# Kernel tuning notes

Measured on AMD Instinct MI355X. Metric: run time of the kernel, lower is better.

The kernel has to match this reference:

```python
import math
import jax, jax.numpy as jnp
import numpy as np

N, L, C_IMG, D, FF, H, NL, V = 2, 1024, 512, 512, 2048, 8, 4, 8000
EPS_ATTN = 1e-6
EPS_LN = 1e-5


def pos_enc(position, channels):
    # position: (N, L, 1) float. channels assumed even here (256 / 512).
    num = channels // 2
    log_inc = math.log(10000.0) / (num - 1)
    inv = jnp.exp(jnp.arange(num, dtype=position.dtype) * -log_inc)
    st = position * inv.reshape(1, 1, -1)  # (N, L, num)
    return jnp.concatenate([jnp.sin(st), jnp.cos(st)], -1)


def layer_norm(x, s, b):
    m = jnp.mean(x, -1, keepdims=True)
    v = jnp.mean((x - m) ** 2, -1, keepdims=True)
    return (x - m) / jnp.sqrt(v + EPS_LN) * s + b


def causal_linear_attention(x, mask, Wq, bq, Wk, bk, Wv, bv, Wo, bo):
    # x: (N, L, D), mask: (N, L, 1)
    n, l, d = x.shape
    q = (x @ Wq + bq).reshape(n, l, H, -1)
    k = (x @ Wk + bk).reshape(n, l, H, -1)
    v = (x @ Wv + bv).reshape(n, l, H, -1)
    Q = jax.nn.elu(q) + 1.0                       # elu feature map
    K = (jax.nn.elu(k) + 1.0) * mask[:, :, :, None]
    K_cum = jnp.cumsum(K, axis=1)                 # (N, L, H, dk)
    Z = 1.0 / (jnp.einsum('nlhd,nlhd->nlh', Q, K_cum) + EPS_ATTN)
    KV = jnp.cumsum(K[..., :, None] * v[..., None, :], axis=1)  # (N, L, H, dk, dv)
    out = jnp.einsum('nlhd,nlhde->nlhe', Q, KV) * Z[..., None]
    return out.reshape(n, l, d) @ Wo + bo


def encoder_layer(x, mask, p):
    (Wq, bq, Wk, bk, Wv, bv, Wo, bo, W1, b1, W2, b2, s1, be1, s2, be2) = p
    x = x + causal_linear_attention(x, mask, Wq, bq, Wk, bk, Wv, bv, Wo, bo)
    x = layer_norm(x, s1, be1)
    y = jax.nn.gelu(x @ W1 + b1, approximate=False) @ W2 + b2
    return layer_norm(x + y, s2, be2)


def setup_inputs() -> dict:
    key = jax.random.key(0)
    ks = iter(jax.random.split(key, 64))

    def p(shape):
        return jax.random.normal(next(ks), shape, dtype=jnp.float32) * 0.02

    x_img = jax.random.normal(next(ks), (N, L, C_IMG), dtype=jnp.float32)
    x_txt = jax.random.randint(next(ks), (N, L), 0, V)
    pos = jnp.broadcast_to(jnp.arange(L, dtype=jnp.float32)[None, :, None], (N, L, 1))
    pos_r = jnp.floor(pos / 32.0)
    pos_c = jnp.mod(pos, 32.0)
    pos_t = pos
    first_half = (jnp.arange(L) < L // 2).astype(jnp.float32)[None, :, None]
    mask_img = jnp.broadcast_to(first_half, (N, L, 1))
    mask_txt = 1.0 - mask_img

    inp = dict(x_img=x_img, x_txt=x_txt, mask_img=mask_img, mask_txt=mask_txt,
               pos_r=pos_r, pos_c=pos_c, pos_t=pos_t,
               W_ei=p((C_IMG, D)), b_ei=jnp.zeros((D,)),
               emb_txt=p((V, D)),
               Wq=p((NL, D, D)), bq=jnp.zeros((NL, D)),
               Wk=p((NL, D, D)), bk=jnp.zeros((NL, D)),
               Wv=p((NL, D, D)), bv=jnp.zeros((NL, D)),
               Wo=p((NL, D, D)), bo=jnp.zeros((NL, D)),
               W1=p((NL, D, FF)), b1=jnp.zeros((NL, FF)),
               W2=p((NL, FF, D)), b2=jnp.zeros((NL, D)),
               ln1_s=jnp.ones((NL, D)), ln1_b=jnp.zeros((NL, D)),
               ln2_s=jnp.ones((NL, D)), ln2_b=jnp.zeros((NL, D)),
               W_pi=p((D, C_IMG)), b_pi=jnp.zeros((C_IMG,)),
               W_pt=p((D, V)), b_pt=jnp.zeros((V,)))
    return inp


def reference(x_img, x_txt, mask_img, mask_txt, pos_r, pos_c, pos_t,
              W_ei, b_ei, emb_txt,
              Wq, bq, Wk, bk, Wv, bv, Wo, bo, W1, b1, W2, b2,
              ln1_s, ln1_b, ln2_s, ln2_b, W_pi, b_pi, W_pt, b_pt):
    x_mask = mask_img + mask_txt  # (N, L, 1)
    # image embedding
    half = D // 2
    x_pos = jnp.concatenate([pos_enc(pos_r, half), pos_enc(pos_c, D - half)], -1)
    x_emb_img = ((x_img @ W_ei + b_ei) + x_pos) * mask_img
    # text embedding
    x_emb_txt = (emb_txt[x_txt] + pos_enc(pos_t, D)) * mask_txt
    x = x_emb_img + x_emb_txt
    for i in range(NL):
        p = (Wq[i], bq[i], Wk[i], bk[i], Wv[i], bv[i], Wo[i], bo[i],
             W1[i], b1[i], W2[i], b2[i], ln1_s[i], ln1_b[i], ln2_s[i], ln2_b[i])
        x = encoder_layer(x, x_mask, p)
    logit_img = x @ W_pi + b_pi
    logit_txt = x @ W_pt + b_pt
    return (logit_img, logit_txt)
```

## Files before the change

### kernel.cpp

```cpp
#include <hip/hip_runtime.h>
#include <hip/hip_bf16.h>
#include <math.h>

#define NB 2
#define LSEQ 1024
#define DM 512
#define FFD 2048
#define NHEAD 8
#define DKH 64
#define NLAYER 4
#define VOCAB 8000
#define NCHUNK 16
#define NROWS (NB * LSEQ)
#define QS 1536
#define NHEADCAT 8512
#define NHEADPAD 8576

#define OP_NONE 0
#define OP_GELU 2
#define OP_QKV  3
#define OP_PART 4
#define OP_HEAD 5

typedef __attribute__((ext_vector_type(8))) short short8;
typedef __attribute__((ext_vector_type(4))) float f32x4;
typedef __hip_bfloat16 bf16;

__device__ __forceinline__ void cast_tile(
    const float* __restrict__ s, bf16* __restrict__ d, int K, int N,
    int n0, int k0, int tid)
{
    __shared__ float tile[32][33];
    const int r  = tid >> 3;
    const int c4 = (tid & 7) * 4;
    const int n  = n0 + c4;
    float4 v = make_float4(0.f, 0.f, 0.f, 0.f);
    if (n < N)
        v = *(const float4*)(s + (size_t)(k0 + r) * N + n);
    tile[r][c4 + 0] = v.x; tile[r][c4 + 1] = v.y;
    tile[r][c4 + 2] = v.z; tile[r][c4 + 3] = v.w;
    __syncthreads();
    const int nr = tid >> 3;
    const int kc = (tid & 7) * 4;
    bf16 o[4];
    o[0] = __float2bfloat16(tile[kc + 0][nr]);
    o[1] = __float2bfloat16(tile[kc + 1][nr]);
    o[2] = __float2bfloat16(tile[kc + 2][nr]);
    o[3] = __float2bfloat16(tile[kc + 3][nr]);
    *(unsigned long long*)(d + (size_t)(n0 + nr) * K + k0 + kc) =
        *(const unsigned long long*)o;
    __syncthreads();
}

#define CO_QKVO 0
#define CO_W1   4096
#define CO_W2   8192
#define CO_WEI  12288
#define CO_WPI  12544
#define CO_WPT  12800
#define CO_XIMG 16832
#define CO_QKVB 17856
#define CO_HB   17860
#define CO_END  17894

__global__ __launch_bounds__(256) void setup_all(
    const float* __restrict__ Wq, const float* __restrict__ Wk,
    const float* __restrict__ Wv, const float* __restrict__ Wo,
    const float* __restrict__ W1, const float* __restrict__ W2,
    const float* __restrict__ Wei, const float* __restrict__ Wpi,
    const float* __restrict__ Wpt,
    bf16* __restrict__ QKVt, bf16* __restrict__ Wot,
    bf16* __restrict__ W1t, bf16* __restrict__ W2t,
    bf16* __restrict__ Weit, bf16* __restrict__ Whead,
    const float* __restrict__ x_img, bf16* __restrict__ ximgh,
    const float* __restrict__ bq, const float* __restrict__ bk,
    const float* __restrict__ bv, float* __restrict__ qkvB,
    const float* __restrict__ bpi, const float* __restrict__ bpt,
    float* __restrict__ hb)
{
    const int id = blockIdx.x;
    const int tid = threadIdx.x;

    if (id < CO_W1) {
        const int rel = id;
        const int z = rel >> 8, t = rel & 255;
        const int layer = z >> 2, which = z & 3;
        const float* src = (which == 0 ? Wq : which == 1 ? Wk : which == 2 ? Wv : Wo)
                           + (size_t)layer * 262144;
        bf16* dst = (which < 3)
            ? (QKVt + (size_t)layer * 786432 + (size_t)which * 262144)
            : (Wot + (size_t)layer * 262144);
        cast_tile(src, dst, 512, 512, (t & 15) * 32, (t >> 4) * 32, tid);
    } else if (id < CO_W2) {
        const int rel = id - CO_W1;
        const int z = rel >> 10, t = rel & 1023;
        cast_tile(W1 + (size_t)z * 1048576, W1t + (size_t)z * 1048576,
                  512, 2048, (t & 63) * 32, (t >> 6) * 32, tid);
    } else if (id < CO_WEI) {
        const int rel = id - CO_W2;
        const int z = rel >> 10, t = rel & 1023;
        cast_tile(W2 + (size_t)z * 1048576, W2t + (size_t)z * 1048576,
                  2048, 512, (t & 15) * 32, (t >> 4) * 32, tid);
    } else if (id < CO_WPI) {
        const int t = id - CO_WEI;
        cast_tile(Wei, Weit, 512, 512, (t & 15) * 32, (t >> 4) * 32, tid);
    } else if (id < CO_WPT) {
        const int t = id - CO_WPI;
        cast_tile(Wpi, Whead, 512, 512, (t & 15) * 32, (t >> 4) * 32, tid);
    } else if (id < CO_XIMG) {
        const int t = id - CO_WPT;
        cast_tile(Wpt, Whead + 262144, 512, VOCAB,
                  (t % 252) * 32, (t / 252) * 32, tid);
    } else if (id < CO_QKVB) {
        const int i = (id - CO_XIMG) * 256 + tid;
        const float4 v = *(const float4*)(x_img + (size_t)i * 4);
        ximgh[(size_t)i * 4 + 0] = __float2bfloat16(v.x);
        ximgh[(size_t)i * 4 + 1] = __float2bfloat16(v.y);
        ximgh[(size_t)i * 4 + 2] = __float2bfloat16(v.z);
        ximgh[(size_t)i * 4 + 3] = __float2bfloat16(v.w);
    } else if (id < CO_HB) {
        const int z = id - CO_QKVB;
        for (int j = tid; j < QS; j += 256) {
            float v;
            if (j < 512)       v = bq[z * DM + j];
            else if (j < 1024) v = bk[z * DM + j - 512];
            else               v = bv[z * DM + j - 1024];
            qkvB[z * QS + j] = v;
        }
    } else {
        const int j = (id - CO_HB) * 256 + tid;
        if (j < NHEADPAD)
            hb[j] = (j < 512) ? bpi[j] : (j < NHEADCAT ? bpt[j - 512] : 0.f);
    }
}

template<int BM, int BN>
__global__ __launch_bounds__(256) void gemm16(
    const bf16* __restrict__ A, const bf16* __restrict__ Bt,
    const float* __restrict__ bias, const float* __restrict__ res,
    float* __restrict__ outF, float* __restrict__ outF2,
    bf16* __restrict__ outH,
    int M, int K, int Nout, int op, int kslab)
{
    constexpr int WM = BM / 2, WN = BN / 2, MI = WM / 16, NI = WN / 16;
    constexpr int LA = BM / 64, LB = BN / 64;
    constexpr int NL = LA + LB;
    __shared__ bf16 As[3][BM * 32];
    __shared__ bf16 Bs[3][BN * 32];
    const int tid = threadIdx.x;
    const int lane = tid & 63;
    const int wave = tid >> 6;
    const int wm = (wave >> 1) * WM, wn = (wave & 1) * WN;

    int bxi = blockIdx.x, byi = blockIdx.y;
    if (op == OP_HEAD) {
        const int gx = gridDim.x;
        const int nwg = gx * gridDim.y;
        int flat = byi * gx + bxi;
        const int q = nwg >> 3, r = nwg & 7;
        const int xcd = flat & 7, lid = flat >> 3;
        flat = (xcd < r ? xcd * (q + 1) : r * (q + 1) + (xcd - r) * q) + lid;
        bxi = flat % gx;
        byi = flat / gx;
    }
    const int bm = (op == OP_HEAD ? bxi : blockIdx.y) * BM;
    const int bn = (op == OP_HEAD ? byi : blockIdx.x) * BN;
    const int l16 = lane & 15, quad = lane >> 4;

    const int rA = tid >> 2;
    const int c8 = (tid & 3) << 3;

    f32x4 acc[MI][NI];
    #pragma unroll
    for (int i = 0; i < MI; ++i)
        #pragma unroll
        for (int j = 0; j < NI; ++j) acc[i][j] = (f32x4){0.f, 0.f, 0.f, 0.f};

    const bf16* gA = A  + (size_t)(bm + rA) * K + c8;
    const bf16* gB = Bt + (size_t)(bn + rA) * K + c8;
    const int ldsWaveOff = wave * 1024;

    const int kStart = blockIdx.z * kslab;
    const int kEnd = kStart + kslab;

    auto stage = [&](int buf, int k0) {
        #pragma unroll
        for (int i = 0; i < LA; ++i)
            __builtin_amdgcn_global_load_lds(
                (const __attribute__((address_space(1))) void*)(gA + (size_t)i * 64 * K + k0),
                (__attribute__((address_space(3))) void*)((char*)As[buf] + i * 4096 + ldsWaveOff),
                16, 0, 0);
        #pragma unroll
        for (int i = 0; i < LB; ++i)
            __builtin_amdgcn_global_load_lds(
                (const __attribute__((address_space(1))) void*)(gB + (size_t)i * 64 * K + k0),
                (__attribute__((address_space(3))) void*)((char*)Bs[buf] + i * 4096 + ldsWaveOff),
                16, 0, 0);
    };

    stage(0, kStart);
    if (kStart + 32 < kEnd) stage(1, kStart + 32);
    int cur = 0;
    for (int k0 = kStart; k0 < kEnd; k0 += 32) {
        const int k2 = k0 + 64;
        if (k2 < kEnd) {
            int nb = cur + 2; if (nb >= 3) nb -= 3;
            stage(nb, k2);
            asm volatile("s_waitcnt vmcnt(%0)" :: "n"(2 * NL) : "memory");
        } else if (k0 + 32 < kEnd) {
            asm volatile("s_waitcnt vmcnt(%0)" :: "n"(NL) : "memory");
        } else {
            asm volatile("s_waitcnt vmcnt(0)" ::: "memory");
        }
        __builtin_amdgcn_s_barrier();
        short8 a[MI], b[NI];
        #pragma unroll
        for (int i = 0; i < MI; ++i)
            a[i] = *(const short8*)(As[cur] + (size_t)(wm + i * 16 + l16) * 32 + quad * 8);
        #pragma unroll
        for (int j = 0; j < NI; ++j)
            b[j] = *(const short8*)(Bs[cur] + (size_t)(wn + j * 16 + l16) * 32 + quad * 8);
        #pragma unroll
        for (int i = 0; i < MI; ++i)
            #pragma unroll
            for (int j = 0; j < NI; ++j)
                acc[i][j] = __builtin_amdgcn_mfma_f32_16x16x32_bf16(
                    a[i], b[j], acc[i][j], 0, 0, 0);
        __builtin_amdgcn_s_barrier();
        ++cur; if (cur >= 3) cur -= 3;
    }

    if (op == OP_PART) {
        float* dst = outF + (size_t)blockIdx.z * (size_t)M * Nout;
        #pragma unroll
        for (int j = 0; j < NI; ++j) {
            const int col = bn + wn + j * 16 + l16;
            #pragma unroll
            for (int i = 0; i < MI; ++i)
                #pragma unroll
                for (int r = 0; r < 4; ++r) {
                    const int row = bm + wm + i * 16 + quad * 4 + r;
                    dst[(size_t)row * Nout + col] = acc[i][j][r];
                }
        }
        return;
    }
    if (op == OP_HEAD) {
        #pragma unroll
        for (int j = 0; j < NI; ++j) {
            const int col = bn + wn + j * 16 + l16;
            const bool cok = (col < NHEADCAT);
            const float bz = cok ? bias[col] : 0.f;
            #pragma unroll
            for (int i = 0; i < MI; ++i)
                #pragma unroll
                for (int r = 0; r < 4; ++r) {
                    const int row = bm + wm + i * 16 + quad * 4 + r;
                    const float v = acc[i][j][r] + bz;
                    if (cok) {
                        if (col < 512) outF[(size_t)row * 512 + col] = v;
                        else           outF2[(size_t)row * VOCAB + (col - 512)] = v;
                    }
                }
        }
        return;
    }

    #pragma unroll
    for (int j = 0; j < NI; ++j) {
        const int col = bn + wn + j * 16 + l16;
        const bool cok = (col < Nout);
        const float bz = cok ? bias[col] : 0.f;
        #pragma unroll
        for (int i = 0; i < MI; ++i) {
            #pragma unroll
            for (int r = 0; r < 4; ++r) {
                const int row = bm + wm + i * 16 + quad * 4 + r;
                float v = acc[i][j][r] + bz;
                if (op == OP_GELU)      v = 0.5f * v * (1.f + erff(v * 0.70710678118654752f));
                else if (op == OP_QKV && col < 1024) v = (v > 0.f) ? v + 1.f : expf(v);
                if (cok) {
                    if (res)  v += res[(size_t)row * Nout + col];
                    if (outF) outF[(size_t)row * Nout + col] = v;
                    if (outH) outH[(size_t)row * Nout + col] = __float2bfloat16(v);
                }
            }
        }
    }
}

__global__ __launch_bounds__(256) void embed_k(
    const float* __restrict__ gI, const int* __restrict__ xt,
    const float* __restrict__ emb,
    const float* __restrict__ mi, const float* __restrict__ mt,
    const float* __restrict__ pr, const float* __restrict__ pc,
    const float* __restrict__ pt, float* __restrict__ X, bf16* __restrict__ Xh)
{
    const int row = blockIdx.x;
    const float prv = pr[row], pcv = pc[row], ptv = pt[row];
    const float miv = mi[row], mtv = mt[row];
    const int tok = xt[row];
    const float LOG1E4 = 9.2103403719761836f;
    const float LI127 = LOG1E4 / 127.f;
    const float LI255 = LOG1E4 / 255.f;

    for (int d = threadIdx.x; d < DM; d += 256) {
        float ip;
        if (d < 128)       ip = sinf(prv * expf(-(float)d * LI127));
        else if (d < 256)  ip = cosf(prv * expf(-(float)(d - 128) * LI127));
        else if (d < 384)  ip = sinf(pcv * expf(-(float)(d - 256) * LI127));
        else               ip = cosf(pcv * expf(-(float)(d - 384) * LI127));
        float tp;
        if (d < 256) tp = sinf(ptv * expf(-(float)d * LI255));
        else         tp = cosf(ptv * expf(-(float)(d - 256) * LI255));
        const float v = miv * (gI[(size_t)row * DM + d] + ip)
                      + mtv * (emb[(size_t)tok * DM + d] + tp);
        X[(size_t)row * DM + d] = v;
        Xh[(size_t)row * DM + d] = __float2bfloat16(v);
    }
}

__global__ __launch_bounds__(256) void ln_red(
    const float* __restrict__ P, int nP,
    const float* __restrict__ bias, const float* __restrict__ res,
    const float* __restrict__ g, const float* __restrict__ b,
    float* __restrict__ out, bf16* __restrict__ outh)
{
    const int row = blockIdx.x;
    const int tid = threadIdx.x;
    const int lane = tid & 63, wv = tid >> 6;
    const size_t base = (size_t)row * DM;
    float x0 = res[base + tid] + bias[tid];
    float x1 = res[base + tid + 256] + bias[tid + 256];
    for (int p = 0; p < nP; ++p) {
        x0 += P[(size_t)p * 1048576 + base + tid];
        x1 += P[(size_t)p * 1048576 + base + tid + 256];
    }
    __shared__ float redA[4];
    __shared__ float redB[4];
    float s = x0 + x1;
    #pragma unroll
    for (int off = 32; off > 0; off >>= 1) s += __shfl_down(s, off);
    if (lane == 0) redA[wv] = s;
    __syncthreads();
    const float mean = (redA[0] + redA[1] + redA[2] + redA[3]) * (1.f / (float)DM);
    const float d0 = x0 - mean, d1 = x1 - mean;
    float v = d0 * d0 + d1 * d1;
    #pragma unroll
    for (int off = 32; off > 0; off >>= 1) v += __shfl_down(v, off);
    if (lane == 0) redB[wv] = v;
    __syncthreads();
    const float var = (redB[0] + redB[1] + redB[2] + redB[3]) * (1.f / (float)DM);
    const float rstd = rsqrtf(var + 1e-5f);
    const float y0 = d0 * rstd * g[tid] + b[tid];
    const float y1 = d1 * rstd * g[tid + 256] + b[tid + 256];
    out[base + tid]        = y0;
    out[base + tid + 256]  = y1;
    outh[base + tid]       = __float2bfloat16(y0);
    outh[base + tid + 256] = __float2bfloat16(y1);
}

__global__ __launch_bounds__(256) void attn_kv(
    const float* __restrict__ Kp, const float* __restrict__ Vp,
    float* __restrict__ S, float* __restrict__ ks)
{
    const int c = blockIdx.x, h = blockIdx.y, n = blockIdx.z;
    const int tid = threadIdx.x;
    __shared__ float sK[64][64], sV[64][64], part[4][64];

    const int lr = tid >> 4;
    const int c4 = (tid & 15) * 4;
    #pragma unroll
    for (int it = 0; it < 4; ++it) {
        const int row = it * 16 + lr;
        const size_t gb = ((size_t)(n * LSEQ + c * 64 + row)) * QS + h * DKH + c4;
        *(float4*)&sK[row][c4] = *(const float4*)(Kp + gb);
        *(float4*)&sV[row][c4] = *(const float4*)(Vp + gb);
    }
    __syncthreads();

    const int e = tid & 63, dq = tid >> 6;
    float s[16] = {};
    for (int l = 0; l < 64; ++l) {
        const float vv = sV[l][e];
        const float4 k0 = *(const float4*)&sK[l][dq * 16 + 0];
        const float4 k1 = *(const float4*)&sK[l][dq * 16 + 4];
        const float4 k2 = *(const float4*)&sK[l][dq * 16 + 8];
        const float4 k3 = *(const float4*)&sK[l][dq * 16 + 12];
        s[0]  = fmaf(k0.x, vv, s[0]);  s[1]  = fmaf(k0.y, vv, s[1]);
        s[2]  = fmaf(k0.z, vv, s[2]);  s[3]  = fmaf(k0.w, vv, s[3]);
        s[4]  = fmaf(k1.x, vv, s[4]);  s[5]  = fmaf(k1.y, vv, s[5]);
        s[6]  = fmaf(k1.z, vv, s[6]);  s[7]  = fmaf(k1.w, vv, s[7]);
        s[8]  = fmaf(k2.x, vv, s[8]);  s[9]  = fmaf(k2.y, vv, s[9]);
        s[10] = fmaf(k2.z, vv, s[10]); s[11] = fmaf(k2.w, vv, s[11]);
        s[12] = fmaf(k3.x, vv, s[12]); s[13] = fmaf(k3.y, vv, s[13]);
        s[14] = fmaf(k3.z, vv, s[14]); s[15] = fmaf(k3.w, vv, s[15]);
    }
    const size_t sb = (((size_t)(n * NHEAD + h)) * NCHUNK + c) * 4096;
    #pragma unroll
    for (int i = 0; i < 16; ++i) S[sb + (size_t)(dq * 16 + i) * 64 + e] = s[i];

    float kp = 0.f;
    #pragma unroll
    for (int i = 0; i < 16; ++i) kp += sK[dq * 16 + i][e];
    part[dq][e] = kp;
    __syncthreads();
    if (tid < 64)
        ks[(((size_t)(n * NHEAD + h)) * NCHUNK + c) * 64 + tid] =
            part[0][tid] + part[1][tid] + part[2][tid] + part[3][tid];
}

__global__ __launch_bounds__(256) void attn_out(
    const float* __restrict__ QKV, const float* __restrict__ S,
    const float* __restrict__ ks, bf16* __restrict__ O)
{
    const int c = blockIdx.x, h = blockIdx.y, n = blockIdx.z;
    const int tid = threadIdx.x;
    __shared__ float sQt[64][64];
    __shared__ float sKt[64][64];
    __shared__ float sV [64][64];
    __shared__ float sS [64][64];
    __shared__ float sPt[64][65];
    __shared__ float skp[64];

    const size_t nhS = ((size_t)(n * NHEAD + h)) * NCHUNK * 4096;
    const size_t nhK = ((size_t)(n * NHEAD + h)) * NCHUNK * 64;

    {
        float4 aS[4] = {};
        for (int cc = 0; cc < c; ++cc) {
            const float* Sc = S + nhS + (size_t)cc * 4096;
            #pragma unroll
            for (int i = 0; i < 4; ++i) {
                const float4 t = *(const float4*)(Sc + i * 1024 + tid * 4);
                aS[i].x += t.x; aS[i].y += t.y; aS[i].z += t.z; aS[i].w += t.w;
            }
        }
        float* sSf = &sS[0][0];
        #pragma unroll
        for (int i = 0; i < 4; ++i)
            *(float4*)(sSf + i * 1024 + tid * 4) = aS[i];
        if (tid < 64) {
            float kp = 0.f;
            for (int cc = 0; cc < c; ++cc) kp += ks[nhK + cc * 64 + tid];
            skp[tid] = kp;
        }
    }

    const int lr = tid >> 4;
    const int c4 = (tid & 15) * 4;
    #pragma unroll
    for (int it = 0; it < 4; ++it) {
        const int row = it * 16 + lr;
        const size_t gb = ((size_t)(n * LSEQ + c * 64 + row)) * QS + h * DKH + c4;
        const float4 q4 = *(const float4*)(QKV + gb);
        const float4 k4 = *(const float4*)(QKV + gb + 512);
        const float4 v4 = *(const float4*)(QKV + gb + 1024);
        sQt[c4 + 0][row] = q4.x; sQt[c4 + 1][row] = q4.y;
        sQt[c4 + 2][row] = q4.z; sQt[c4 + 3][row] = q4.w;
        sKt[c4 + 0][row] = k4.x; sKt[c4 + 1][row] = k4.y;
        sKt[c4 + 2][row] = k4.z; sKt[c4 + 3][row] = k4.w;
        *(float4*)&sV[row][c4] = v4;
    }
    __syncthreads();

    const int m4 = (tid & 15) * 4;
    const int lg = tid >> 4;
    {
        float p[4][4] = {};
        for (int d = 0; d < 64; ++d) {
            const float4 k4 = *(const float4*)&sKt[d][m4];
            const float4 q4 = *(const float4*)&sQt[d][lg * 4];
            p[0][0] = fmaf(q4.x, k4.x, p[0][0]); p[0][1] = fmaf(q4.x, k4.y, p[0][1]);
            p[0][2] = fmaf(q4.x, k4.z, p[0][2]); p[0][3] = fmaf(q4.x, k4.w, p[0][3]);
            p[1][0] = fmaf(q4.y, k4.x, p[1][0]); p[1][1] = fmaf(q4.y, k4.y, p[1][1]);
            p[1][2] = fmaf(q4.y, k4.z, p[1][2]); p[1][3] = fmaf(q4.y, k4.w, p[1][3]);
            p[2][0] = fmaf(q4.z, k4.x, p[2][0]); p[2][1] = fmaf(q4.z, k4.y, p[2][1]);
            p[2][2] = fmaf(q4.z, k4.z, p[2][2]); p[2][3] = fmaf(q4.z, k4.w, p[2][3]);
            p[3][0] = fmaf(q4.w, k4.x, p[3][0]); p[3][1] = fmaf(q4.w, k4.y, p[3][1]);
            p[3][2] = fmaf(q4.w, k4.z, p[3][2]); p[3][3] = fmaf(q4.w, k4.w, p[3][3]);
        }
        #pragma unroll
        for (int jj = 0; jj < 4; ++jj)
            #pragma unroll
            for (int j = 0; j < 4; ++j)
                sPt[m4 + jj][lg * 4 + j] = p[j][jj];
    }
    __syncthreads();

    float acc[4][4] = {};
    float z[4] = {};
    const int lmax = lg * 4 + 3;
    for (int m = 0; m <= lmax; ++m) {
        const float4 v4 = *(const float4*)&sV[m][m4];
        #pragma unroll
        for (int j = 0; j < 4; ++j) {
            const int l = lg * 4 + j;
            float p = sPt[m][l];
            p = (m <= l) ? p : 0.f;
            z[j] += p;
            acc[j][0] = fmaf(p, v4.x, acc[j][0]);
            acc[j][1] = fmaf(p, v4.y, acc[j][1]);
            acc[j][2] = fmaf(p, v4.z, acc[j][2]);
            acc[j][3] = fmaf(p, v4.w, acc[j][3]);
        }
    }
    for (int d = 0; d < 64; ++d) {
        const float4 s4 = *(const float4*)&sS[d][m4];
        const float4 q4 = *(const float4*)&sQt[d][lg * 4];
        const float kp = skp[d];
        z[0] = fmaf(q4.x, kp, z[0]); z[1] = fmaf(q4.y, kp, z[1]);
        z[2] = fmaf(q4.z, kp, z[2]); z[3] = fmaf(q4.w, kp, z[3]);
        acc[0][0] = fmaf(q4.x, s4.x, acc[0][0]); acc[0][1] = fmaf(q4.x, s4.y, acc[0][1]);
        acc[0][2] = fmaf(q4.x, s4.z, acc[0][2]); acc[0][3] = fmaf(q4.x, s4.w, acc[0][3]);
        acc[1][0] = fmaf(q4.y, s4.x, acc[1][0]); acc[1][1] = fmaf(q4.y, s4.y, acc[1][1]);
        acc[1][2] = fmaf(q4.y, s4.z, acc[1][2]); acc[1][3] = fmaf(q4.y, s4.w, acc[1][3]);
        acc[2][0] = fmaf(q4.z, s4.x, acc[2][0]); acc[2][1] = fmaf(q4.z, s4.y, acc[2][1]);
        acc[2][2] = fmaf(q4.z, s4.z, acc[2][2]); acc[2][3] = fmaf(q4.z, s4.w, acc[2][3]);
        acc[3][0] = fmaf(q4.w, s4.x, acc[3][0]); acc[3][1] = fmaf(q4.w, s4.y, acc[3][1]);
        acc[3][2] = fmaf(q4.w, s4.z, acc[3][2]); acc[3][3] = fmaf(q4.w, s4.w, acc[3][3]);
    }
    #pragma unroll
    for (int j = 0; j < 4; ++j) {
        const int l = lg * 4 + j;
        const float rz = 1.f / (z[j] + 1e-6f);
        const size_t ob = ((size_t)(n * LSEQ + c * 64 + l)) * DM + h * DKH + m4;
        O[ob + 0] = __float2bfloat16(acc[j][0] * rz);
        O[ob + 1] = __float2bfloat16(acc[j][1] * rz);
        O[ob + 2] = __float2bfloat16(acc[j][2] * rz);
        O[ob + 3] = __float2bfloat16(acc[j][3] * rz);
    }
}

extern "C" void kernel_launch(void* const* d_in, const int* in_sizes, int n_in,
                              void* d_out, int out_size, void* d_ws, size_t ws_size,
                              hipStream_t stream)
{
    const float* x_img   = (const float*)d_in[0];
    const int*   x_txt   = (const int*)  d_in[1];
    const float* mask_i  = (const float*)d_in[2];
    const float* mask_t  = (const float*)d_in[3];
    const float* pos_r   = (const float*)d_in[4];
    const float* pos_c   = (const float*)d_in[5];
    const float* pos_t   = (const float*)d_in[6];
    const float* W_ei    = (const float*)d_in[7];
    const float* b_ei    = (const float*)d_in[8];
    const float* emb_txt = (const float*)d_in[9];
    const float* Wq      = (const float*)d_in[10];
    const float* bq      = (const float*)d_in[11];
    const float* Wk      = (const float*)d_in[12];
    const float* bk      = (const float*)d_in[13];
    const float* Wv      = (const float*)d_in[14];
    const float* bv      = (const float*)d_in[15];
    const float* Wo      = (const float*)d_in[16];
    const float* bo      = (const float*)d_in[17];
    const float* W1      = (const float*)d_in[18];
    const float* b1      = (const float*)d_in[19];
    const float* W2      = (const float*)d_in[20];
    const float* b2      = (const float*)d_in[21];
    const float* ln1_s   = (const float*)d_in[22];
    const float* ln1_b   = (const float*)d_in[23];
    const float* ln2_s   = (const float*)d_in[24];
    const float* ln2_b   = (const float*)d_in[25];
    const float* W_pi    = (const float*)d_in[26];
    const float* b_pi    = (const float*)d_in[27];
    const float* W_pt    = (const float*)d_in[28];
    const float* b_pt    = (const float*)d_in[29];

    float* ws = (float*)d_ws;
    size_t off = 0;
    auto alloc = [&](size_t nfloats) { float* p = ws + off; off += nfloats; return p; };

    float* Xb   = alloc(1048576);
    float* Pb   = alloc(4194304);
    float* QKVb = alloc(3145728);
    float* Sb   = alloc(1048576);
    float* ksb  = alloc(16384);
    float* qkvB = alloc(4 * QS);
    float* hb   = alloc(8704);
    bf16* Xh    = (bf16*)alloc(524288);
    bf16* Ob    = (bf16*)alloc(524288);
    bf16* Tb    = (bf16*)alloc(2097152);
    bf16* ximgh = (bf16*)alloc(524288);
    bf16* QKVt  = (bf16*)alloc(1572864);
    bf16* Wot   = (bf16*)alloc(524288);
    bf16* W1t   = (bf16*)alloc(2097152);
    bf16* W2t   = (bf16*)alloc(2097152);
    bf16* Weit  = (bf16*)alloc(131072);
    bf16* Whead = (bf16*)alloc(2195456);

    const dim3 blk(256);
    const dim3 gAttn(NCHUNK, NHEAD, NB);

    setup_all<<<dim3(CO_END), blk, 0, stream>>>(
        Wq, Wk, Wv, Wo, W1, W2, W_ei, W_pi, W_pt,
        QKVt, Wot, W1t, W2t, Weit, Whead,
        x_img, ximgh, bq, bk, bv, qkvB, b_pi, b_pt, hb);

    gemm16<64, 64><<<dim3(8, 32), blk, 0, stream>>>(
        ximgh, Weit, b_ei, nullptr, Pb, nullptr, nullptr, NROWS, 512, 512, OP_NONE, 512);
    embed_k<<<NROWS, blk, 0, stream>>>(Pb, x_txt, emb_txt, mask_i, mask_t,
                                       pos_r, pos_c, pos_t, Xb, Xh);

    for (int i = 0; i < NLAYER; ++i) {
        gemm16<64, 128><<<dim3(12, 32), blk, 0, stream>>>(
            Xh, QKVt + (size_t)i * 786432, qkvB + i * QS, nullptr,
            QKVb, nullptr, nullptr, NROWS, 512, QS, OP_QKV, 512);

        attn_kv<<<gAttn, blk, 0, stream>>>(QKVb + 512, QKVb + 1024, Sb, ksb);
        attn_out<<<gAttn, blk, 0, stream>>>(QKVb, Sb, ksb, Ob);

        gemm16<64, 64><<<dim3(8, 32, 2), blk, 0, stream>>>(
            Ob, Wot + (size_t)i * 262144, nullptr, nullptr,
            Pb, nullptr, nullptr, NROWS, 512, 512, OP_PART, 256);
        ln_red<<<NROWS, blk, 0, stream>>>(Pb, 2, bo + (size_t)i * DM, Xb,
                                          ln1_s + (size_t)i * DM,
                                          ln1_b + (size_t)i * DM, Xb, Xh);

        gemm16<64, 128><<<dim3(16, 32), blk, 0, stream>>>(
            Xh, W1t + (size_t)i * 1048576, b1 + (size_t)i * FFD, nullptr,
            nullptr, nullptr, Tb, NROWS, 512, FFD, OP_GELU, 512);
        gemm16<64, 64><<<dim3(8, 32, 4), blk, 0, stream>>>(
            Tb, W2t + (size_t)i * 1048576, nullptr, nullptr,
            Pb, nullptr, nullptr, NROWS, 2048, 512, OP_PART, 512);
        ln_red<<<NROWS, blk, 0, stream>>>(Pb, 4, b2 + (size_t)i * DM, Xb,
                                          ln2_s + (size_t)i * DM,
                                          ln2_b + (size_t)i * DM, Xb, Xh);
    }

    float* out = (float*)d_out;
    gemm16<128, 128><<<dim3(16, 67), blk, 0, stream>>>(
        Xh, Whead, hb, nullptr, out, out + 1048576, nullptr,
        NROWS, 512, NHEADCAT, OP_HEAD, 512);
}
```

Before: 631.1 us.

## Replace 4-wave GEMM with single-wave 64x64 GEMM using swizzled LDS double buffering

Replaces the templated 256-thread GEMM with a single-wave 64x64 tile kernel. It uses a two-buffer LDS pipeline with no workgroup barriers and XOR-swizzled LDS addressing to avoid bank conflicts. Grids are rescaled so every GEMM, including the head, uses 64x64 tiles, giving many more small blocks. This removes barrier overhead and aims for higher occupancy, at the cost of less tile reuse (more global and L2 traffic) for the larger tiles it replaces.

```diff
diff --git a/kernel.cpp b/kernel.cpp
--- a/kernel.cpp
+++ b/kernel.cpp
@@ -134,67 +134,67 @@
     }
 }
 
-template<int BM, int BN>
-__global__ __launch_bounds__(256) void gemm16(
+__global__ __launch_bounds__(64) void wgemm(
     const bf16* __restrict__ A, const bf16* __restrict__ Bt,
     const float* __restrict__ bias, const float* __restrict__ res,
     float* __restrict__ outF, float* __restrict__ outF2,
     bf16* __restrict__ outH,
     int M, int K, int Nout, int op, int kslab)
 {
-    constexpr int WM = BM / 2, WN = BN / 2, MI = WM / 16, NI = WN / 16;
-    constexpr int LA = BM / 64, LB = BN / 64;
-    constexpr int NL = LA + LB;
-    __shared__ bf16 As[3][BM * 32];
-    __shared__ bf16 Bs[3][BN * 32];
-    const int tid = threadIdx.x;
-    const int lane = tid & 63;
-    const int wave = tid >> 6;
-    const int wm = (wave >> 1) * WM, wn = (wave & 1) * WN;
-
-    int bxi = blockIdx.x, byi = blockIdx.y;
+    __shared__ bf16 As[2][64 * 32];
+    __shared__ bf16 Bs[2][64 * 32];
+    const int lane = threadIdx.x;
+    const int l16 = lane & 15, quad = lane >> 4;
+    const int rr = lane >> 2;
+    const int sl = lane & 3;
+
+    int bm, bn;
     if (op == OP_HEAD) {
         const int gx = gridDim.x;
         const int nwg = gx * gridDim.y;
-        int flat = byi * gx + bxi;
+        int flat = blockIdx.y * gx + blockIdx.x;
         const int q = nwg >> 3, r = nwg & 7;
         const int xcd = flat & 7, lid = flat >> 3;
         flat = (xcd < r ? xcd * (q + 1) : r * (q + 1) + (xcd - r) * q) + lid;
-        bxi = flat % gx;
-        byi = flat / gx;
-    }
-    const int bm = (op == OP_HEAD ? bxi : blockIdx.y) * BM;
-    const int bn = (op == OP_HEAD ? byi : blockIdx.x) * BN;
-    const int l16 = lane & 15, quad = lane >> 4;
-
-    const int rA = tid >> 2;
-    const int c8 = (tid & 3) << 3;
-
-    f32x4 acc[MI][NI];
-    #pragma unroll
-    for (int i = 0; i < MI; ++i)
-        #pragma unroll
-        for (int j = 0; j < NI; ++j) acc[i][j] = (f32x4){0.f, 0.f, 0.f, 0.f};
-
-    const bf16* gA = A  + (size_t)(bm + rA) * K + c8;
-    const bf16* gB = Bt + (size_t)(bn + rA) * K + c8;
-    const int ldsWaveOff = wave * 1024;
+        bm = (flat % gx) * 64;
+        bn = (flat / gx) * 64;
+    } else {
+        bm = blockIdx.y * 64;
+        bn = blockIdx.x * 64;
+    }
+
+    f32x4 acc[4][4];
+    #pragma unroll
+    for (int i = 0; i < 4; ++i)
+        #pragma unroll
+        for (int j = 0; j < 4; ++j) acc[i][j] = (f32x4){0.f, 0.f, 0.f, 0.f};
+
+    const int csw = (sl ^ ((rr >> 1) & 3)) << 3;
+    const int rsw = ((quad ^ ((l16 >> 1) & 3)) << 3);
+
+    const bf16* gA[4];
+    const bf16* gB[4];
+    #pragma unroll
+    for (int i = 0; i < 4; ++i) {
+        gA[i] = A  + (size_t)(bm + i * 16 + rr) * K + csw;
+        gB[i] = Bt + (size_t)(bn + i * 16 + rr) * K + csw;
+    }
 
     const int kStart = blockIdx.z * kslab;
     const int kEnd = kStart + kslab;
 
     auto stage = [&](int buf, int k0) {
         #pragma unroll
-        for (int i = 0; i < LA; ++i)
+        for (int i = 0; i < 4; ++i)
             __builtin_amdgcn_global_load_lds(
-                (const __attribute__((address_space(1))) void*)(gA + (size_t)i * 64 * K + k0),
-                (__attribute__((address_space(3))) void*)((char*)As[buf] + i * 4096 + ldsWaveOff),
+                (const __attribute__((address_space(1))) void*)(gA[i] + k0),
+                (__attribute__((address_space(3))) void*)((char*)As[buf] + i * 1024),
                 16, 0, 0);
         #pragma unroll
-        for (int i = 0; i < LB; ++i)
+        for (int i = 0; i < 4; ++i)
             __builtin_amdgcn_global_load_lds(
-                (const __attribute__((address_space(1))) void*)(gB + (size_t)i * 64 * K + k0),
-                (__attribute__((address_space(3))) void*)((char*)Bs[buf] + i * 4096 + ldsWaveOff),
+                (const __attribute__((address_space(1))) void*)(gB[i] + k0),
+                (__attribute__((address_space(3))) void*)((char*)Bs[buf] + i * 1024),
                 16, 0, 0);
     };
 
@@ -202,44 +202,38 @@
     if (kStart + 32 < kEnd) stage(1, kStart + 32);
     int cur = 0;
     for (int k0 = kStart; k0 < kEnd; k0 += 32) {
-        const int k2 = k0 + 64;
-        if (k2 < kEnd) {
-            int nb = cur + 2; if (nb >= 3) nb -= 3;
-            stage(nb, k2);
-            asm volatile("s_waitcnt vmcnt(%0)" :: "n"(2 * NL) : "memory");
-        } else if (k0 + 32 < kEnd) {
-            asm volatile("s_waitcnt vmcnt(%0)" :: "n"(NL) : "memory");
-        } else {
+        if (k0 + 32 < kEnd)
+            asm volatile("s_waitcnt vmcnt(8)" ::: "memory");
+        else
             asm volatile("s_waitcnt vmcnt(0)" ::: "memory");
-        }
-        __builtin_amdgcn_s_barrier();
-        short8 a[MI], b[NI];
-        #pragma unroll
-        for (int i = 0; i < MI; ++i)
-            a[i] = *(const short8*)(As[cur] + (size_t)(wm + i * 16 + l16) * 32 + quad * 8);
-        #pragma unroll
-        for (int j = 0; j < NI; ++j)
-            b[j] = *(const short8*)(Bs[cur] + (size_t)(wn + j * 16 + l16) * 32 + quad * 8);
-        #pragma unroll
-        for (int i = 0; i < MI; ++i)
+        short8 a[4], b[4];
+        #pragma unroll
+        for (int i = 0; i < 4; ++i)
+            a[i] = *(const short8*)(As[cur] + (i * 16 + l16) * 32 + rsw);
+        #pragma unroll
+        for (int j = 0; j < 4; ++j)
+            b[j] = *(const short8*)(Bs[cur] + (j * 16 + l16) * 32 + rsw);
+        asm volatile("s_waitcnt lgkmcnt(0)" ::: "memory");
+        if (k0 + 64 < kEnd) stage(cur, k0 + 64);
+        #pragma unroll
+        for (int i = 0; i < 4; ++i)
             #pragma unroll
-            for (int j = 0; j < NI; ++j)
+            for (int j = 0; j < 4; ++j)
                 acc[i][j] = __builtin_amdgcn_mfma_f32_16x16x32_bf16(
                     a[i], b[j], acc[i][j], 0, 0, 0);
-        __builtin_amdgcn_s_barrier();
-        ++cur; if (cur >= 3) cur -= 3;
+        cur ^= 1;
     }
 
     if (op == OP_PART) {
         float* dst = outF + (size_t)blockIdx.z * (size_t)M * Nout;
         #pragma unroll
-        for (int j = 0; j < NI; ++j) {
-            const int col = bn + wn + j * 16 + l16;
+        for (int j = 0; j < 4; ++j) {
+            const int col = bn + j * 16 + l16;
             #pragma unroll
-            for (int i = 0; i < MI; ++i)
+            for (int i = 0; i < 4; ++i)
                 #pragma unroll
                 for (int r = 0; r < 4; ++r) {
-                    const int row = bm + wm + i * 16 + quad * 4 + r;
+                    const int row = bm + i * 16 + quad * 4 + r;
                     dst[(size_t)row * Nout + col] = acc[i][j][r];
                 }
         }
@@ -247,15 +241,15 @@
     }
     if (op == OP_HEAD) {
         #pragma unroll
-        for (int j = 0; j < NI; ++j) {
-            const int col = bn + wn + j * 16 + l16;
+        for (int j = 0; j < 4; ++j) {
+            const int col = bn + j * 16 + l16;
             const bool cok = (col < NHEADCAT);
             const float bz = cok ? bias[col] : 0.f;
             #pragma unroll
-            for (int i = 0; i < MI; ++i)
+            for (int i = 0; i < 4; ++i)
                 #pragma unroll
                 for (int r = 0; r < 4; ++r) {
-                    const int row = bm + wm + i * 16 + quad * 4 + r;
+                    const int row = bm + i * 16 + quad * 4 + r;
                     const float v = acc[i][j][r] + bz;
                     if (cok) {
                         if (col < 512) outF[(size_t)row * 512 + col] = v;
@@ -267,15 +261,15 @@
     }
 
     #pragma unroll
-    for (int j = 0; j < NI; ++j) {
-        const int col = bn + wn + j * 16 + l16;
+    for (int j = 0; j < 4; ++j) {
+        const int col = bn + j * 16 + l16;
         const bool cok = (col < Nout);
         const float bz = cok ? bias[col] : 0.f;
         #pragma unroll
-        for (int i = 0; i < MI; ++i) {
+        for (int i = 0; i < 4; ++i) {
             #pragma unroll
             for (int r = 0; r < 4; ++r) {
-                const int row = bm + wm + i * 16 + quad * 4 + r;
+                const int row = bm + i * 16 + quad * 4 + r;
                 float v = acc[i][j][r] + bz;
                 if (op == OP_GELU)      v = 0.5f * v * (1.f + erff(v * 0.70710678118654752f));
                 else if (op == OP_QKV && col < 1024) v = (v > 0.f) ? v + 1.f : expf(v);
@@ -590,6 +584,7 @@
     bf16* Whead = (bf16*)alloc(2195456);
 
     const dim3 blk(256);
+    const dim3 wblk(64);
     const dim3 gAttn(NCHUNK, NHEAD, NB);
 
     setup_all<<<dim3(CO_END), blk, 0, stream>>>(
@@ -597,30 +592,30 @@
         QKVt, Wot, W1t, W2t, Weit, Whead,
         x_img, ximgh, bq, bk, bv, qkvB, b_pi, b_pt, hb);
 
-    gemm16<64, 64><<<dim3(8, 32), blk, 0, stream>>>(
+    wgemm<<<dim3(8, 32), wblk, 0, stream>>>(
         ximgh, Weit, b_ei, nullptr, Pb, nullptr, nullptr, NROWS, 512, 512, OP_NONE, 512);
     embed_k<<<NROWS, blk, 0, stream>>>(Pb, x_txt, emb_txt, mask_i, mask_t,
                                        pos_r, pos_c, pos_t, Xb, Xh);
 
     for (int i = 0; i < NLAYER; ++i) {
-        gemm16<64, 128><<<dim3(12, 32), blk, 0, stream>>>(
+        wgemm<<<dim3(24, 32), wblk, 0, stream>>>(
             Xh, QKVt + (size_t)i * 786432, qkvB + i * QS, nullptr,
             QKVb, nullptr, nullptr, NROWS, 512, QS, OP_QKV, 512);
 
         attn_kv<<<gAttn, blk, 0, stream>>>(QKVb + 512, QKVb + 1024, Sb, ksb);
         attn_out<<<gAttn, blk, 0, stream>>>(QKVb, Sb, ksb, Ob);
 
-        gemm16<64, 64><<<dim3(8, 32, 2), blk, 0, stream>>>(
+        wgemm<<<dim3(8, 32, 2), wblk, 0, stream>>>(
             Ob, Wot + (size_t)i * 262144, nullptr, nullptr,
             Pb, nullptr, nullptr, NROWS, 512, 512, OP_PART, 256);
         ln_red<<<NROWS, blk, 0, stream>>>(Pb, 2, bo + (size_t)i * DM, Xb,
                                           ln1_s + (size_t)i * DM,
                                           ln1_b + (size_t)i * DM, Xb, Xh);
 
-        gemm16<64, 128><<<dim3(16, 32), blk, 0, stream>>>(
+        wgemm<<<dim3(32, 32), wblk, 0, stream>>>(
             Xh, W1t + (size_t)i * 1048576, b1 + (size_t)i * FFD, nullptr,
             nullptr, nullptr, Tb, NROWS, 512, FFD, OP_GELU, 512);
-        gemm16<64, 64><<<dim3(8, 32, 4), blk, 0, stream>>>(
+        wgemm<<<dim3(8, 32, 4), wblk, 0, stream>>>(
             Tb, W2t + (size_t)i * 1048576, nullptr, nullptr,
             Pb, nullptr, nullptr, NROWS, 2048, 512, OP_PART, 512);
         ln_red<<<NROWS, blk, 0, stream>>>(Pb, 4, b2 + (size_t)i * DM, Xb,
@@ -629,7 +624,7 @@
     }
 
     float* out = (float*)d_out;
-    gemm16<128, 128><<<dim3(16, 67), blk, 0, stream>>>(
+    wgemm<<<dim3(32, 134), wblk, 0, stream>>>(
         Xh, Whead, hb, nullptr, out, out + 1048576, nullptr,
         NROWS, 512, NHEADCAT, OP_HEAD, 512);
 }
```

Result: slower. 674.1 us (+6.8%).

## Replace layer GEMMs with single-wave 32x32 tile kernel with swizzled LDS

Applied to the files above, without the earlier changes.

Adds a new one-wave-per-block GEMM (32x32 tiles, double-buffered global_load_lds with an XOR swizzle for LDS bank conflicts, no block barriers) and uses it for the embedding, QKV, output-projection and FFN GEMMs. The 256-thread gemm16 is reduced to the head-only path and changes from triple to double buffering. The aim is more workgroups to fill the CUs and less barrier overhead on these small GEMMs. In exchange each block reuses operands much less, so global/L2 traffic per FLOP goes up, and the head GEMM loses a stage of prefetch.

```diff
diff --git a/kernel.cpp b/kernel.cpp
--- a/kernel.cpp
+++ b/kernel.cpp
@@ -137,34 +137,33 @@
 template<int BM, int BN>
 __global__ __launch_bounds__(256) void gemm16(
     const bf16* __restrict__ A, const bf16* __restrict__ Bt,
-    const float* __restrict__ bias, const float* __restrict__ res,
+    const float* __restrict__ bias,
     float* __restrict__ outF, float* __restrict__ outF2,
-    bf16* __restrict__ outH,
-    int M, int K, int Nout, int op, int kslab)
+    int M, int K, int Nout, int kslab)
 {
     constexpr int WM = BM / 2, WN = BN / 2, MI = WM / 16, NI = WN / 16;
     constexpr int LA = BM / 64, LB = BN / 64;
     constexpr int NL = LA + LB;
-    __shared__ bf16 As[3][BM * 32];
-    __shared__ bf16 Bs[3][BN * 32];
+    __shared__ bf16 As[2][BM * 32];
+    __shared__ bf16 Bs[2][BN * 32];
     const int tid = threadIdx.x;
     const int lane = tid & 63;
     const int wave = tid >> 6;
     const int wm = (wave >> 1) * WM, wn = (wave & 1) * WN;
 
-    int bxi = blockIdx.x, byi = blockIdx.y;
-    if (op == OP_HEAD) {
+    int bxi, byi;
+    {
         const int gx = gridDim.x;
         const int nwg = gx * gridDim.y;
-        int flat = byi * gx + bxi;
+        int flat = blockIdx.y * gx + blockIdx.x;
         const int q = nwg >> 3, r = nwg & 7;
         const int xcd = flat & 7, lid = flat >> 3;
         flat = (xcd < r ? xcd * (q + 1) : r * (q + 1) + (xcd - r) * q) + lid;
         bxi = flat % gx;
         byi = flat / gx;
     }
-    const int bm = (op == OP_HEAD ? bxi : blockIdx.y) * BM;
-    const int bn = (op == OP_HEAD ? byi : blockIdx.x) * BN;
+    const int bm = bxi * BM;
+    const int bn = byi * BN;
     const int l16 = lane & 15, quad = lane >> 4;
 
     const int rA = tid >> 2;
@@ -180,8 +179,8 @@
     const bf16* gB = Bt + (size_t)(bn + rA) * K + c8;
     const int ldsWaveOff = wave * 1024;
 
-    const int kStart = blockIdx.z * kslab;
-    const int kEnd = kStart + kslab;
+    const int kStart = 0;
+    const int kEnd = kslab;
 
     auto stage = [&](int buf, int k0) {
         #pragma unroll
@@ -199,15 +198,11 @@
     };
 
     stage(0, kStart);
-    if (kStart + 32 < kEnd) stage(1, kStart + 32);
     int cur = 0;
     for (int k0 = kStart; k0 < kEnd; k0 += 32) {
-        const int k2 = k0 + 64;
-        if (k2 < kEnd) {
-            int nb = cur + 2; if (nb >= 3) nb -= 3;
-            stage(nb, k2);
-            asm volatile("s_waitcnt vmcnt(%0)" :: "n"(2 * NL) : "memory");
-        } else if (k0 + 32 < kEnd) {
+        const bool hasNext = (k0 + 32 < kEnd);
+        if (hasNext) {
+            stage(cur ^ 1, k0 + 32);
             asm volatile("s_waitcnt vmcnt(%0)" :: "n"(NL) : "memory");
         } else {
             asm volatile("s_waitcnt vmcnt(0)" ::: "memory");
@@ -227,63 +222,133 @@
                 acc[i][j] = __builtin_amdgcn_mfma_f32_16x16x32_bf16(
                     a[i], b[j], acc[i][j], 0, 0, 0);
         __builtin_amdgcn_s_barrier();
-        ++cur; if (cur >= 3) cur -= 3;
+        cur ^= 1;
+    }
+
+    #pragma unroll
+    for (int j = 0; j < NI; ++j) {
+        const int col = bn + wn + j * 16 + l16;
+        const bool cok = (col < NHEADCAT);
+        const float bz = cok ? bias[col] : 0.f;
+        #pragma unroll
+        for (int i = 0; i < MI; ++i)
+            #pragma unroll
+            for (int r = 0; r < 4; ++r) {
+                const int row = bm + wm + i * 16 + quad * 4 + r;
+                const float v = acc[i][j][r] + bz;
+                if (cok) {
+                    if (col < 512) outF[(size_t)row * 512 + col] = v;
+                    else           outF2[(size_t)row * VOCAB + (col - 512)] = v;
+                }
+            }
+    }
+}
+
+__global__ __launch_bounds__(64) void wgemm32(
+    const bf16* __restrict__ A, const bf16* __restrict__ Bt,
+    const float* __restrict__ bias,
+    float* __restrict__ outF, bf16* __restrict__ outH,
+    int M, int K, int Nout, int op, int kslab)
+{
+    __shared__ bf16 As[2][32 * 32];
+    __shared__ bf16 Bs[2][32 * 32];
+    const int lane = threadIdx.x;
+    const int l16 = lane & 15, quad = lane >> 4;
+    const int bm = blockIdx.y * 32;
+    const int bn = blockIdx.x * 32;
+
+    f32x4 acc[2][2];
+    #pragma unroll
+    for (int i = 0; i < 2; ++i)
+        #pragma unroll
+        for (int j = 0; j < 2; ++j) acc[i][j] = (f32x4){0.f, 0.f, 0.f, 0.f};
+
+    const int rr  = lane >> 2;
+    const int csw = ((lane & 3) ^ ((lane >> 3) & 3)) << 3;
+    const int rsw = (quad ^ ((l16 >> 1) & 3)) << 3;
+
+    const bf16* gA[2];
+    const bf16* gB[2];
+    #pragma unroll
+    for (int i = 0; i < 2; ++i) {
+        gA[i] = A  + (size_t)(bm + i * 16 + rr) * K + csw;
+        gB[i] = Bt + (size_t)(bn + i * 16 + rr) * K + csw;
+    }
+
+    const int kStart = blockIdx.z * kslab;
+    const int kEnd = kStart + kslab;
+
+    auto stage = [&](int buf, int k0) {
+        #pragma unroll
+        for (int i = 0; i < 2; ++i)
+            __builtin_amdgcn_global_load_lds(
+                (const __attribute__((address_space(1))) void*)(gA[i] + k0),
+                (__attribute__((address_space(3))) void*)((char*)As[buf] + i * 1024),
+                16, 0, 0);
+        #pragma unroll
+        for (int i = 0; i < 2; ++i)
+            __builtin_amdgcn_global_load_lds(
+                (const __attribute__((address_space(1))) void*)(gB[i] + k0),
+                (__attribute__((address_space(3))) void*)((char*)Bs[buf] + i * 1024),
+                16, 0, 0);
+    };
+
+    stage(0, kStart);
+    if (kStart + 32 < kEnd) stage(1, kStart + 32);
+    int cur = 0;
+    for (int k0 = kStart; k0 < kEnd; k0 += 32) {
+        if (k0 + 32 < kEnd)
+            asm volatile("s_waitcnt vmcnt(4)" ::: "memory");
+        else
+            asm volatile("s_waitcnt vmcnt(0)" ::: "memory");
+        short8 a[2], b[2];
+        #pragma unroll
+        for (int i = 0; i < 2; ++i)
+            a[i] = *(const short8*)(As[cur] + (i * 16 + l16) * 32 + rsw);
+        #pragma unroll
+        for (int j = 0; j < 2; ++j)
+            b[j] = *(const short8*)(Bs[cur] + (j * 16 + l16) * 32 + rsw);
+        asm volatile("s_waitcnt lgkmcnt(0)" ::: "memory");
+        if (k0 + 64 < kEnd) stage(cur, k0 + 64);
+        #pragma unroll
+        for (int i = 0; i < 2; ++i)
+            #pragma unroll
+            for (int j = 0; j < 2; ++j)
+                acc[i][j] = __builtin_amdgcn_mfma_f32_16x16x32_bf16(
+                    a[i], b[j], acc[i][j], 0, 0, 0);
+        cur ^= 1;
     }
 
     if (op == OP_PART) {
         float* dst = outF + (size_t)blockIdx.z * (size_t)M * Nout;
         #pragma unroll
-        for (int j = 0; j < NI; ++j) {
-            const int col = bn + wn + j * 16 + l16;
+        for (int j = 0; j < 2; ++j) {
+            const int col = bn + j * 16 + l16;
             #pragma unroll
-            for (int i = 0; i < MI; ++i)
+            for (int i = 0; i < 2; ++i)
                 #pragma unroll
                 for (int r = 0; r < 4; ++r) {
-                    const int row = bm + wm + i * 16 + quad * 4 + r;
+                    const int row = bm + i * 16 + quad * 4 + r;
                     dst[(size_t)row * Nout + col] = acc[i][j][r];
                 }
         }
         return;
     }
-    if (op == OP_HEAD) {
-        #pragma unroll
-        for (int j = 0; j < NI; ++j) {
-            const int col = bn + wn + j * 16 + l16;
-            const bool cok = (col < NHEADCAT);
-            const float bz = cok ? bias[col] : 0.f;
-            #pragma unroll
-            for (int i = 0; i < MI; ++i)
-                #pragma unroll
-                for (int r = 0; r < 4; ++r) {
-                    const int row = bm + wm + i * 16 + quad * 4 + r;
-                    const float v = acc[i][j][r] + bz;
-                    if (cok) {
-                        if (col < 512) outF[(size_t)row * 512 + col] = v;
-                        else           outF2[(size_t)row * VOCAB + (col - 512)] = v;
-                    }
-                }
-        }
-        return;
-    }
-
-    #pragma unroll
-    for (int j = 0; j < NI; ++j) {
-        const int col = bn + wn + j * 16 + l16;
-        const bool cok = (col < Nout);
-        const float bz = cok ? bias[col] : 0.f;
-        #pragma unroll
-        for (int i = 0; i < MI; ++i) {
+
+    #pragma unroll
+    for (int j = 0; j < 2; ++j) {
+        const int col = bn + j * 16 + l16;
+        const float bz = bias ? bias[col] : 0.f;
+        #pragma unroll
+        for (int i = 0; i < 2; ++i) {
             #pragma unroll
             for (int r = 0; r < 4; ++r) {
-                const int row = bm + wm + i * 16 + quad * 4 + r;
+                const int row = bm + i * 16 + quad * 4 + r;
                 float v = acc[i][j][r] + bz;
                 if (op == OP_GELU)      v = 0.5f * v * (1.f + erff(v * 0.70710678118654752f));
                 else if (op == OP_QKV && col < 1024) v = (v > 0.f) ? v + 1.f : expf(v);
-                if (cok) {
-                    if (res)  v += res[(size_t)row * Nout + col];
-                    if (outF) outF[(size_t)row * Nout + col] = v;
-                    if (outH) outH[(size_t)row * Nout + col] = __float2bfloat16(v);
-                }
+                if (outF) outF[(size_t)row * Nout + col] = v;
+                if (outH) outH[(size_t)row * Nout + col] = __float2bfloat16(v);
             }
         }
     }
@@ -590,6 +655,7 @@
     bf16* Whead = (bf16*)alloc(2195456);
 
     const dim3 blk(256);
+    const dim3 wblk(64);
     const dim3 gAttn(NCHUNK, NHEAD, NB);
 
     setup_all<<<dim3(CO_END), blk, 0, stream>>>(
@@ -597,32 +663,32 @@
         QKVt, Wot, W1t, W2t, Weit, Whead,
         x_img, ximgh, bq, bk, bv, qkvB, b_pi, b_pt, hb);
 
-    gemm16<64, 64><<<dim3(8, 32), blk, 0, stream>>>(
-        ximgh, Weit, b_ei, nullptr, Pb, nullptr, nullptr, NROWS, 512, 512, OP_NONE, 512);
+    wgemm32<<<dim3(16, 64), wblk, 0, stream>>>(
+        ximgh, Weit, b_ei, Pb, nullptr, NROWS, 512, 512, OP_NONE, 512);
     embed_k<<<NROWS, blk, 0, stream>>>(Pb, x_txt, emb_txt, mask_i, mask_t,
                                        pos_r, pos_c, pos_t, Xb, Xh);
 
     for (int i = 0; i < NLAYER; ++i) {
-        gemm16<64, 128><<<dim3(12, 32), blk, 0, stream>>>(
-            Xh, QKVt + (size_t)i * 786432, qkvB + i * QS, nullptr,
-            QKVb, nullptr, nullptr, NROWS, 512, QS, OP_QKV, 512);
+        wgemm32<<<dim3(48, 64), wblk, 0, stream>>>(
+            Xh, QKVt + (size_t)i * 786432, qkvB + i * QS,
+            QKVb, nullptr, NROWS, 512, QS, OP_QKV, 512);
 
         attn_kv<<<gAttn, blk, 0, stream>>>(QKVb + 512, QKVb + 1024, Sb, ksb);
         attn_out<<<gAttn, blk, 0, stream>>>(QKVb, Sb, ksb, Ob);
 
-        gemm16<64, 64><<<dim3(8, 32, 2), blk, 0, stream>>>(
-            Ob, Wot + (size_t)i * 262144, nullptr, nullptr,
-            Pb, nullptr, nullptr, NROWS, 512, 512, OP_PART, 256);
+        wgemm32<<<dim3(16, 64, 2), wblk, 0, stream>>>(
+            Ob, Wot + (size_t)i * 262144, nullptr,
+            Pb, nullptr, NROWS, 512, 512, OP_PART, 256);
         ln_red<<<NROWS, blk, 0, stream>>>(Pb, 2, bo + (size_t)i * DM, Xb,
                                           ln1_s + (size_t)i * DM,
                                           ln1_b + (size_t)i * DM, Xb, Xh);
 
-        gemm16<64, 128><<<dim3(16, 32), blk, 0, stream>>>(
-            Xh, W1t + (size_t)i * 1048576, b1 + (size_t)i * FFD, nullptr,
-            nullptr, nullptr, Tb, NROWS, 512, FFD, OP_GELU, 512);
-        gemm16<64, 64><<<dim3(8, 32, 4), blk, 0, stream>>>(
-            Tb, W2t + (size_t)i * 1048576, nullptr, nullptr,
-            Pb, nullptr, nullptr, NROWS, 2048, 512, OP_PART, 512);
+        wgemm32<<<dim3(64, 64), wblk, 0, stream>>>(
+            Xh, W1t + (size_t)i * 1048576, b1 + (size_t)i * FFD,
+            nullptr, Tb, NROWS, 512, FFD, OP_GELU, 512);
+        wgemm32<<<dim3(16, 64, 4), wblk, 0, stream>>>(
+            Tb, W2t + (size_t)i * 1048576, nullptr,
+            Pb, nullptr, NROWS, 2048, 512, OP_PART, 512);
         ln_red<<<NROWS, blk, 0, stream>>>(Pb, 4, b2 + (size_t)i * DM, Xb,
                                           ln2_s + (size_t)i * DM,
                                           ln2_b + (size_t)i * DM, Xb, Xh);
@@ -630,6 +696,5 @@
 
     float* out = (float*)d_out;
     gemm16<128, 128><<<dim3(16, 67), blk, 0, stream>>>(
-        Xh, Whead, hb, nullptr, out, out + 1048576, nullptr,
-        NROWS, 512, NHEADCAT, OP_HEAD, 512);
-}
+        Xh, Whead, hb, out, out + 1048576, NROWS, 512, NHEADCAT, 512);
+}
```

After: 642.0 us. No clear change (+1.7%).
